# Kernel tuning notes

Hardware: AMD Instinct MI355X
Metric: run time of the kernel (lower is better)

## Reference

```python
import jax, jax.numpy as jnp
import numpy as np

LEAK = 0.2
NUM_GRAPHS = 64


def _gat(h_in, src, dst, eh, W, att_src, att_dst, att_edge, lin_edge_W, bias, N):
    # PyG GATConv with edge_dim, concat=False (mean over heads)
    H, C = att_src.shape
    h = (h_in @ W).reshape(N, H, C)                      # [N,H,C]
    e = (eh @ lin_edge_W).reshape(-1, H, C)              # [Eaug,H,C]
    a_s = jnp.einsum('nhc,hc->nh', h, att_src)           # [N,H]
    a_d = jnp.einsum('nhc,hc->nh', h, att_dst)
    a_e = jnp.einsum('ehc,hc->eh', e, att_edge)          # [Eaug,H]
    score = jax.nn.leaky_relu(a_s[src] + a_d[dst] + a_e, LEAK)
    # scatter-softmax over incoming edges of each destination node
    m = jax.ops.segment_max(score, dst, num_segments=N)
    ex = jnp.exp(score - m[dst])
    den = jax.ops.segment_sum(ex, dst, num_segments=N)
    alpha = ex / den[dst]                                # [Eaug,H]
    out = jax.ops.segment_sum(alpha[:, :, None] * h[src], dst, num_segments=N)
    return out.mean(axis=1) + bias                       # concat=False -> head mean


def setup_inputs() -> dict:
    key = jax.random.key(0)
    ks = jax.random.split(key, 32)
    N, E, F, FE, HID, H, NT = 30000, 480000, 64, 16, 64, 4, 16
    Cin1 = F + HID
    s = 0.05
    d = {
        'x': jax.random.normal(ks[0], (N, F), jnp.float32),
        'edge_attr': jax.random.normal(ks[1], (E, FE), jnp.float32),
        'node_emb': jax.random.normal(ks[2], (NT, HID), jnp.float32) * s,
        'edge_W': jax.random.normal(ks[3], (FE, HID), jnp.float32) * s,
        'edge_b': jnp.zeros((HID,), jnp.float32),
        'W1': jax.random.normal(ks[4], (Cin1, H * HID), jnp.float32) * s,
        'as1': jax.random.normal(ks[5], (H, HID), jnp.float32) * s,
        'ad1': jax.random.normal(ks[6], (H, HID), jnp.float32) * s,
        'ae1': jax.random.normal(ks[7], (H, HID), jnp.float32) * s,
        'leW1': jax.random.normal(ks[8], (HID, H * HID), jnp.float32) * s,
        'b1': jnp.zeros((HID,), jnp.float32),
        'W2': jax.random.normal(ks[9], (HID, H * HID), jnp.float32) * s,
        'as2': jax.random.normal(ks[10], (H, HID), jnp.float32) * s,
        'ad2': jax.random.normal(ks[11], (H, HID), jnp.float32) * s,
        'ae2': jax.random.normal(ks[12], (H, HID), jnp.float32) * s,
        'leW2': jax.random.normal(ks[13], (HID, H * HID), jnp.float32) * s,
        'b2': jnp.zeros((HID,), jnp.float32),
        'sage_Wl': jax.random.normal(ks[14], (HID, HID), jnp.float32) * s,
        'sage_bl': jnp.zeros((HID,), jnp.float32),
        'sage_Wr': jax.random.normal(ks[15], (HID, HID), jnp.float32) * s,
        'lin1_W': jax.random.normal(ks[16], (HID, HID), jnp.float32) * s,
        'lin1_b': jnp.zeros((HID,), jnp.float32),
        'lin2_W': jax.random.normal(ks[17], (HID, HID), jnp.float32) * s,
        'lin2_b': jnp.zeros((HID,), jnp.float32),
        'tel_W': jax.random.normal(ks[18], (HID, 1), jnp.float32) * s,
        'tel_b': jnp.zeros((1,), jnp.float32),
        'comp_W': jax.random.normal(ks[19], (HID, 1), jnp.float32) * s,
        'comp_b': jnp.zeros((1,), jnp.float32),
        'pch_W': jax.random.normal(ks[20], (HID, 1), jnp.float32) * s,
        'pch_b': jnp.zeros((1,), jnp.float32),
        'edge_index': jax.random.randint(ks[21], (2, E), 0, N, jnp.int32),
        'batch': jnp.sort(jax.random.randint(ks[22], (N,), 0, NUM_GRAPHS, jnp.int32)),
        'node_type': jax.random.randint(ks[23], (N,), 0, NT, jnp.int32),
    }
    return d


def reference(x, edge_attr, node_emb, edge_W, edge_b,
              W1, as1, ad1, ae1, leW1, b1,
              W2, as2, ad2, ae2, leW2, b2,
              sage_Wl, sage_bl, sage_Wr,
              lin1_W, lin1_b, lin2_W, lin2_b,
              tel_W, tel_b, comp_W, comp_b, pch_W, pch_b,
              edge_index, batch, node_type):
    N = x.shape[0]
    src0, dst0 = edge_index[0], edge_index[1]

    h0 = jnp.concatenate([x, node_emb[node_type]], axis=-1)   # [N, F+HID]
    eh = edge_attr @ edge_W + edge_b                          # [E, HID]

    # GATConv default add_self_loops=True, fill_value='mean' on edge_attr
    loop = jnp.arange(N, dtype=src0.dtype)
    src = jnp.concatenate([src0, loop])
    dst = jnp.concatenate([dst0, loop])
    eh_aug = jnp.concatenate([eh, jnp.broadcast_to(eh.mean(axis=0), (N, eh.shape[1]))], axis=0)

    h1 = jax.nn.elu(_gat(h0, src, dst, eh_aug, W1, as1, ad1, ae1, leW1, b1, N))
    h2 = jax.nn.elu(_gat(h1, src, dst, eh_aug, W2, as2, ad2, ae2, leW2, b2, N))

    # SAGEConv: mean neighbor aggregation (src->dst) + root transform
    deg = jax.ops.segment_sum(jnp.ones_like(dst0, dtype=h2.dtype), dst0, num_segments=N)
    agg = jax.ops.segment_sum(h2[src0], dst0, num_segments=N) / jnp.clip(deg, 1.0)[:, None]
    h3 = jax.nn.elu(agg @ sage_Wl + sage_bl + h2 @ sage_Wr)

    # global mean pool per graph
    cnt = jax.ops.segment_sum(jnp.ones((N,), h3.dtype), batch, num_segments=NUM_GRAPHS)
    g = jax.ops.segment_sum(h3, batch, num_segments=NUM_GRAPHS) / jnp.clip(cnt, 1.0)[:, None]

    g = jax.nn.elu(g @ lin1_W + lin1_b)                       # dropout inactive (eval)
    g = g @ lin2_W + lin2_b
    return (g @ tel_W + tel_b, g @ comp_W + comp_b, g @ pch_W + pch_b)
```

## Files before the change

kernel.cpp:

```cpp
#include <hip/hip_runtime.h>
#include <math.h>

#define NN 30000
#define NE 480000
#define FEA 16
#define HID 64
#define NG 64
#define LEAKK 0.2f

#define S_AEL1   0
#define S_AEL2   4
#define S_KF1    16
#define S_C1     80
#define S_KF2    88
#define S_C2     152
#define S_MS1    160
#define S_MD1    672
#define S_MS2    1184
#define S_MD2    1440

#define BT1H 0
#define BT1L 20480
#define BT2H 40960
#define BT2L 57344
#define BT3H 73728
#define BT3L 81920

typedef __attribute__((ext_vector_type(8))) short short8;
typedef __attribute__((ext_vector_type(4))) float f32x4;

__device__ __forceinline__ float eluf(float v) { return v > 0.f ? v : expm1f(v); }
__device__ __forceinline__ float leakyf(float v) { return v >= 0.f ? v : LEAKK * v; }
__device__ __forceinline__ void fma4(float4& a, float w, const float4& x) {
    a.x += w * x.x; a.y += w * x.y; a.z += w * x.z; a.w += w * x.w;
}
__device__ __forceinline__ unsigned bf16pack(float a, float b) {
    unsigned ua = __float_as_uint(a), ub = __float_as_uint(b);
    ua = (ua + 0x7FFFu + ((ua >> 16) & 1u)) >> 16;
    ub = (ub + 0x7FFFu + ((ub >> 16) & 1u)) >> 16;
    return ua | (ub << 16);
}
__device__ __forceinline__ unsigned short bf1(float v) {
    unsigned u = __float_as_uint(v);
    return (unsigned short)((u + 0x7FFFu + ((u >> 16) & 1u)) >> 16);
}
__device__ __forceinline__ float bf1tof(unsigned short h) {
    return __uint_as_float(((unsigned)h) << 16);
}
__device__ __forceinline__ uint2 bfpack4(float a, float b, float c, float d) {
    return make_uint2(bf16pack(a, b), bf16pack(c, d));
}
__device__ __forceinline__ float4 bf16x4(uint2 p) {
    float4 r;
    r.x = __uint_as_float(p.x << 16);
    r.y = __uint_as_float(p.x & 0xFFFF0000u);
    r.z = __uint_as_float(p.y << 16);
    r.w = __uint_as_float(p.y & 0xFFFF0000u);
    return r;
}
__device__ __forceinline__ float4 escore4(float4 a, float4 b, float4 c) {
    float4 r;
    r.x = expf(leakyf(a.x + b.x + c.x));
    r.y = expf(leakyf(a.y + b.y + c.y));
    r.z = expf(leakyf(a.z + b.z + c.z));
    r.w = expf(leakyf(a.w + b.w + c.w));
    return r;
}

__global__ __launch_bounds__(256) void cm_prepw_kernel(
    const int* __restrict__ dst, int* __restrict__ cnt, int* __restrict__ rank,
    const float* __restrict__ W1, const float* __restrict__ W2,
    const float* __restrict__ Wl, const float* __restrict__ Wr,
    const float* __restrict__ emb,
    const float* __restrict__ leW1, const float* __restrict__ aew1,
    const float* __restrict__ leW2, const float* __restrict__ aew2,
    const float* __restrict__ edge_W, const float* __restrict__ edge_b,
    const float* __restrict__ as1, const float* __restrict__ ad1,
    const float* __restrict__ as2, const float* __restrict__ ad2,
    const int* __restrict__ batch,
    unsigned short* __restrict__ BT,
    float* __restrict__ S, int* __restrict__ goff) {
    int t = threadIdx.x, bx = blockIdx.x;
    if (bx < 176) {
        int i = bx * 256 + t;
        float v = 0.f;
        int dsti = -1;
        if (i < 16384) {
            int kk = i >> 6, c = i & 63;
            int h = kk >> 6, k = kk & 63;
            v = 0.25f * W1[k * 256 + h * 64 + c];
            dsti = BT1H + c * 320 + kk;
        } else if (i < 20480) {
            int j2 = i - 16384;
            int r2 = j2 >> 6, c = j2 & 63;
            int tau = r2 >> 2, h = r2 & 3;
            float acc = 0.f;
            for (int j = 0; j < 64; j++)
                acc += emb[tau * 64 + j] * W1[(64 + j) * 256 + h * 64 + c];
            v = 0.25f * acc;
            dsti = BT1H + c * 320 + 256 + r2;
        } else if (i < 36864) {
            int j = i - 20480;
            int kk = j >> 6, c = j & 63;
            int h = kk >> 6, k = kk & 63;
            v = 0.25f * W2[k * 256 + h * 64 + c];
            dsti = BT2H + c * 256 + kk;
        } else if (i < 45056) {
            int j = i - 36864;
            int k = j >> 6, c = j & 63;
            v = (k < 64) ? Wl[k * 64 + c] : Wr[(k - 64) * 64 + c];
            dsti = BT3H + c * 128 + k;
        }
        if (dsti >= 0) {
            unsigned short hi = bf1(v);
            unsigned short lo = bf1(v - bf1tof(hi));
            BT[dsti] = hi;
            BT[dsti + 20480 - ((dsti >= BT2H) ? ((dsti >= BT3H) ? 12288 : 4096) : 0)] = lo;
        }
        return;
    }
    if (bx < 178) {
        int i = (bx - 176) * 256 + t;
        int k = i >> 2, h = i & 3;
        float s = 0.f, d = 0.f;
        for (int c = 0; c < 64; c++) {
            float w = W1[k * 256 + h * 64 + c];
            s += w * as1[h * 64 + c];
            d += w * ad1[h * 64 + c];
        }
        S[S_MS1 + i] = s; S[S_MD1 + i] = d;
        return;
    }
    if (bx == 178) {
        int k = t >> 2, h = t & 3;
        float s = 0.f, d = 0.f;
        for (int c = 0; c < 64; c++) {
            float w = W2[k * 256 + h * 64 + c];
            s += w * as2[h * 64 + c];
            d += w * ad2[h * 64 + c];
        }
        S[S_MS2 + t] = s; S[S_MD2 + t] = d;
        return;
    }
    if (bx == 179) {
        __shared__ float M1s[256], M2s[256];
        {
            int k = t >> 2, h = t & 3;
            float m1 = 0.f, m2 = 0.f;
            for (int c = 0; c < 64; c++) {
                m1 += leW1[k * 256 + h * 64 + c] * aew1[h * 64 + c];
                m2 += leW2[k * 256 + h * 64 + c] * aew2[h * 64 + c];
            }
            M1s[t] = m1; M2s[t] = m2;
        }
        __syncthreads();
        if (t < 64) {
            int f = t >> 2, h = t & 3;
            float k1 = 0.f, k2 = 0.f;
            for (int k = 0; k < 64; k++) {
                k1 += edge_W[f * 64 + k] * M1s[k * 4 + h];
                k2 += edge_W[f * 64 + k] * M2s[k * 4 + h];
            }
            S[S_KF1 + t] = k1; S[S_KF2 + t] = k2;
        } else if (t < 68) {
            int h = t - 64;
            float c1 = 0.f, c2 = 0.f;
            for (int k = 0; k < 64; k++) {
                c1 += edge_b[k] * M1s[k * 4 + h];
                c2 += edge_b[k] * M2s[k * 4 + h];
            }
            S[S_C1 + h] = c1; S[S_C2 + h] = c2;
        }
        return;
    }
    if (bx == 180) {
        if (t > NG) return;
        int lo = 0, hi = NN;
        while (lo < hi) {
            int mid = (lo + hi) >> 1;
            if (batch[mid] < t) lo = mid + 1; else hi = mid;
        }
        goff[t] = lo;
        return;
    }
    int e = (bx - 181) * 256 + t;
    if (e < NE) rank[e] = atomicAdd(&cnt[dst[e]], 1);
}

__global__ void scan_blocks_kernel(const int* __restrict__ cnt, int* __restrict__ eoff,
                                   int* __restrict__ bsum) {
    __shared__ int wsum[16];
    int t = threadIdx.x;
    int i = blockIdx.x * 1024 + t;
    int v = (i < NN) ? cnt[i] : 0;
    int lane = t & 63;
    int incl = v;
#pragma unroll
    for (int ofs = 1; ofs < 64; ofs <<= 1) {
        int u = __shfl_up(incl, ofs, 64);
        if (lane >= ofs) incl += u;
    }
    int wid = t >> 6;
    if (lane == 63) wsum[wid] = incl;
    __syncthreads();
    if (t < 16) {
        int s = wsum[t];
#pragma unroll
        for (int ofs = 1; ofs < 16; ofs <<= 1) {
            int u = __shfl_up(s, ofs, 64);
            if (t >= ofs) s += u;
        }
        wsum[t] = s;
    }
    __syncthreads();
    int excl = incl - v + (wid > 0 ? wsum[wid - 1] : 0);
    if (i < NN) eoff[i] = excl;
    if (t == 1023) bsum[blockIdx.x] = excl + v;
}

__global__ __launch_bounds__(256) void scanadd_attn_kernel(
    const int* __restrict__ bsum, int* __restrict__ eoff,
    const float* __restrict__ x, const float* __restrict__ node_emb,
    const int* __restrict__ node_type, const float* __restrict__ S,
    float* __restrict__ as_, float* __restrict__ ad_, unsigned* __restrict__ xb) {
    __shared__ float xt[64 * 132];
    __shared__ float ms[512], md[512];
    __shared__ int ntS[64];
    int t = threadIdx.x;
    if (blockIdx.x < 118) {
        int j = blockIdx.x >> 2;
        int pref = 0;
        for (int u = 0; u < j; u++) pref += bsum[u];
        int i = blockIdx.x * 256 + t;
        if (i < NN) eoff[i] += pref;
        if (i == 0) eoff[NN] = NE;
        return;
    }
    int n0 = (blockIdx.x - 118) * 64;
    if (t < 64) {
        int n = n0 + t;
        ntS[t] = (n < NN) ? node_type[n] : 0;
    }
    for (int i = t; i < 512; i += 256) { ms[i] = S[S_MS1 + i]; md[i] = S[S_MD1 + i]; }
    __syncthreads();
    for (int i = t; i < 1024; i += 256) {
        int r = i >> 4, c4 = (i & 15) * 4;
        int n = n0 + r;
        float4 f = {0, 0, 0, 0};
        if (n < NN) f = *(const float4*)(x + (size_t)n * 64 + c4);
        *(float4*)&xt[r * 132 + c4] = f;
    }
    for (int i = t; i < 1024; i += 256) {
        int r = i >> 4, c4 = (i & 15) * 4;
        int n = n0 + r;
        float4 f = {0, 0, 0, 0};
        if (n < NN) f = *(const float4*)(node_emb + (size_t)ntS[r] * 64 + c4);
        *(float4*)&xt[r * 132 + 64 + c4] = f;
    }
    __syncthreads();
    for (int i = t; i < 2048; i += 256) {
        int r = i >> 5, u = i & 31;
        int n = n0 + r;
        if (n < NN)
            xb[(size_t)n * 32 + u] = bf16pack(xt[r * 132 + 2 * u], xt[r * 132 + 2 * u + 1]);
    }
    int r = t >> 2, h = t & 3;
    float s = 0.f, d = 0.f;
#pragma unroll 8
    for (int k = 0; k < 128; k++) {
        float xv = xt[r * 132 + k];
        s += xv * ms[k * 4 + h];
        d += xv * md[k * 4 + h];
    }
    int n = n0 + r;
    if (n < NN) { as_[n * 4 + h] = s; ad_[n * 4 + h] = d; }
}

__global__ __launch_bounds__(256) void scatter_proj_kernel(
    const int* __restrict__ src, const int* __restrict__ dst,
    const float* __restrict__ EA, const float* __restrict__ S,
    const float* __restrict__ as_, const float* __restrict__ ad_,
    const int* __restrict__ node_type,
    const int* __restrict__ eoff, const int* __restrict__ rank,
    int* __restrict__ sep, int* __restrict__ dsrt,
    float4* __restrict__ sc1st, float4* __restrict__ ae2st,
    float* __restrict__ Ssum) {
    __shared__ float KF1s[64], KF2s[64], Cs[8];
    __shared__ float red[32];
    int t = threadIdx.x;
    if (t < 64) { KF1s[t] = S[S_KF1 + t]; KF2s[t] = S[S_KF2 + t]; }
    else if (t < 72) { int q = t - 64; Cs[q] = (q < 4) ? S[S_C1 + q] : S[S_C2 + q - 4]; }
    __syncthreads();
    int e = blockIdx.x * 256 + t;
    int s = src[e], d = dst[e];
    float a1[4], a2[4];
#pragma unroll
    for (int h = 0; h < 4; h++) { a1[h] = Cs[h]; a2[h] = Cs[4 + h]; }
    const float4* EA4 = (const float4*)(EA + (size_t)e * FEA);
#pragma unroll
    for (int q = 0; q < 4; q++) {
        float4 v = EA4[q];
        float vv[4] = {v.x, v.y, v.z, v.w};
#pragma unroll
        for (int j = 0; j < 4; j++) {
            int f = q * 4 + j;
#pragma unroll
            for (int h = 0; h < 4; h++) {
                a1[h] += vv[j] * KF1s[f * 4 + h];
                a2[h] += vv[j] * KF2s[f * 4 + h];
            }
        }
    }
    int pos = eoff[d] + rank[e];
    sep[pos] = s | (node_type[s] << 16);
    dsrt[pos] = d;
    float4 asv = ((const float4*)as_)[s];
    float4 adv = ((const float4*)ad_)[d];
    sc1st[pos] = escore4(asv, adv, make_float4(a1[0], a1[1], a1[2], a1[3]));
    ae2st[pos] = make_float4(a2[0], a2[1], a2[2], a2[3]);
    float v[8] = {a1[0], a1[1], a1[2], a1[3], a2[0], a2[1], a2[2], a2[3]};
#pragma unroll
    for (int mask = 1; mask < 64; mask <<= 1)
#pragma unroll
        for (int j = 0; j < 8; j++) v[j] += __shfl_xor(v[j], mask, 64);
    int lane = t & 63, wid = t >> 6;
    if (lane == 0)
#pragma unroll
        for (int j = 0; j < 8; j++) red[wid * 8 + j] = v[j];
    __syncthreads();
    if (t < 8) atomicAdd(&Ssum[t], red[t] + red[8 + t] + red[16 + t] + red[24 + t]);
}

__global__ __launch_bounds__(256) void score2_kernel(
    const int* __restrict__ sep, const int* __restrict__ dsrt,
    const float* __restrict__ as_, const float* __restrict__ ad_,
    float4* __restrict__ ae2st) {
    int p = blockIdx.x * 256 + threadIdx.x;
    int s = sep[p] & 0xFFFF;
    int d = dsrt[p];
    ae2st[p] = escore4(((const float4*)as_)[s], ((const float4*)ad_)[d], ae2st[p]);
}

__global__ __launch_bounds__(256) void agg_gat1_kernel(
    const int* __restrict__ eoff, const int* __restrict__ sep,
    const float* __restrict__ scs, const unsigned* __restrict__ xb,
    const int* __restrict__ node_type,
    const float* __restrict__ as_, const float* __restrict__ ad_,
    const float* __restrict__ S, uint2* __restrict__ aggb) {
    int n = blockIdx.x * 4 + (threadIdx.x >> 6);
    if (n >= NN) return;
    int lane = threadIdx.x & 63;
    int sub = lane >> 4, ch = lane & 15;
    const uint2* Xb = (const uint2*)xb;
    const float4* W4 = (const float4*)scs;
    float4 asn = ((const float4*)as_)[n];
    float4 adn = ((const float4*)ad_)[n];
    float4 a0 = {0, 0, 0, 0}, a1 = a0, a2 = a0, a3 = a0, dn = a0, tw = a0;
    int b = eoff[n], e_end = eoff[n + 1];
    int nE = e_end - b;
    int i = sub;
    for (; i + 4 < nE; i += 8) {
        int p0 = b + i, p1 = p0 + 4;
        int q0 = sep[p0], q1 = sep[p1];
        int s0 = q0 & 0xFFFF, t0 = q0 >> 16;
        int s1 = q1 & 0xFFFF, t1 = q1 >> 16;
        float4 w0 = W4[p0], w1 = W4[p1];
        float4 x0 = bf16x4(Xb[(size_t)s0 * 16 + ch]);
        float4 x1 = bf16x4(Xb[(size_t)s1 * 16 + ch]);
        fma4(a0, w0.x, x0); fma4(a1, w0.y, x0); fma4(a2, w0.z, x0); fma4(a3, w0.w, x0);
        fma4(a0, w1.x, x1); fma4(a1, w1.y, x1); fma4(a2, w1.z, x1); fma4(a3, w1.w, x1);
        dn.x += w0.x + w1.x; dn.y += w0.y + w1.y;
        dn.z += w0.z + w1.z; dn.w += w0.w + w1.w;
        if (ch == t0) { tw.x += w0.x; tw.y += w0.y; tw.z += w0.z; tw.w += w0.w; }
        if (ch == t1) { tw.x += w1.x; tw.y += w1.y; tw.z += w1.z; tw.w += w1.w; }
    }
    for (; i < nE; i += 4) {
        int p0 = b + i;
        int q0 = sep[p0];
        int s0 = q0 & 0xFFFF, t0 = q0 >> 16;
        float4 w0 = W4[p0];
        float4 x0 = bf16x4(Xb[(size_t)s0 * 16 + ch]);
        fma4(a0, w0.x, x0); fma4(a1, w0.y, x0); fma4(a2, w0.z, x0); fma4(a3, w0.w, x0);
        dn.x += w0.x; dn.y += w0.y; dn.z += w0.z; dn.w += w0.w;
        if (ch == t0) { tw.x += w0.x; tw.y += w0.y; tw.z += w0.z; tw.w += w0.w; }
    }
    if (sub == 0) {
        const float inv = 1.f / (float)NE;
        float e0 = expf(leakyf(asn.x + adn.x + S[S_AEL1 + 0] * inv));
        float e1 = expf(leakyf(asn.y + adn.y + S[S_AEL1 + 1] * inv));
        float e2 = expf(leakyf(asn.z + adn.z + S[S_AEL1 + 2] * inv));
        float e3 = expf(leakyf(asn.w + adn.w + S[S_AEL1 + 3] * inv));
        float4 xs = bf16x4(Xb[(size_t)n * 16 + ch]);
        fma4(a0, e0, xs); fma4(a1, e1, xs); fma4(a2, e2, xs); fma4(a3, e3, xs);
        dn.x += e0; dn.y += e1; dn.z += e2; dn.w += e3;
        int tn = node_type[n];
        if (ch == tn) { tw.x += e0; tw.y += e1; tw.z += e2; tw.w += e3; }
    }
#pragma unroll
    for (int mask = 16; mask < 64; mask <<= 1) {
        a0.x += __shfl_xor(a0.x, mask, 64); a0.y += __shfl_xor(a0.y, mask, 64);
        a0.z += __shfl_xor(a0.z, mask, 64); a0.w += __shfl_xor(a0.w, mask, 64);
        a1.x += __shfl_xor(a1.x, mask, 64); a1.y += __shfl_xor(a1.y, mask, 64);
        a1.z += __shfl_xor(a1.z, mask, 64); a1.w += __shfl_xor(a1.w, mask, 64);
        a2.x += __shfl_xor(a2.x, mask, 64); a2.y += __shfl_xor(a2.y, mask, 64);
        a2.z += __shfl_xor(a2.z, mask, 64); a2.w += __shfl_xor(a2.w, mask, 64);
        a3.x += __shfl_xor(a3.x, mask, 64); a3.y += __shfl_xor(a3.y, mask, 64);
        a3.z += __shfl_xor(a3.z, mask, 64); a3.w += __shfl_xor(a3.w, mask, 64);
        dn.x += __shfl_xor(dn.x, mask, 64); dn.y += __shfl_xor(dn.y, mask, 64);
        dn.z += __shfl_xor(dn.z, mask, 64); dn.w += __shfl_xor(dn.w, mask, 64);
        tw.x += __shfl_xor(tw.x, mask, 64); tw.y += __shfl_xor(tw.y, mask, 64);
        tw.z += __shfl_xor(tw.z, mask, 64); tw.w += __shfl_xor(tw.w, mask, 64);
    }
    if (sub == 0) {
        float i0 = 1.f / dn.x, i1 = 1.f / dn.y, i2 = 1.f / dn.z, i3 = 1.f / dn.w;
        uint2* A2 = aggb + (size_t)n * 80;
        A2[ch]      = bfpack4(a0.x * i0, a0.y * i0, a0.z * i0, a0.w * i0);
        A2[16 + ch] = bfpack4(a1.x * i1, a1.y * i1, a1.z * i1, a1.w * i1);
        A2[32 + ch] = bfpack4(a2.x * i2, a2.y * i2, a2.z * i2, a2.w * i2);
        A2[48 + ch] = bfpack4(a3.x * i3, a3.y * i3, a3.z * i3, a3.w * i3);
        A2[64 + ch] = bfpack4(tw.x * i0, tw.y * i1, tw.z * i2, tw.w * i3);
    }
}

__global__ __launch_bounds__(256) void agg_gat2_kernel(
    const int* __restrict__ eoff, const int* __restrict__ sep,
    const float* __restrict__ w2s, const unsigned* __restrict__ h1b,
    const float* __restrict__ as_, const float* __restrict__ ad_,
    const float* __restrict__ S, uint2* __restrict__ aggb) {
    int n = blockIdx.x * 4 + (threadIdx.x >> 6);
    if (n >= NN) return;
    int lane = threadIdx.x & 63;
    int sub = lane >> 4, ch = lane & 15;
    const uint2* Xb = (const uint2*)h1b;
    const float4* W4 = (const float4*)w2s;
    float4 asn = ((const float4*)as_)[n];
    float4 adn = ((const float4*)ad_)[n];
    float4 a0 = {0, 0, 0, 0}, a1 = a0, a2 = a0, a3 = a0, dn = a0;
    int b = eoff[n], e = eoff[n + 1];
    int nE = e - b;
    int i = sub;
    for (; i + 4 < nE; i += 8) {
        int p0 = b + i, p1 = p0 + 4;
        int s0 = sep[p0] & 0xFFFF, s1 = sep[p1] & 0xFFFF;
        float4 w0 = W4[p0], w1 = W4[p1];
        float4 x0 = bf16x4(Xb[(size_t)s0 * 16 + ch]);
        float4 x1 = bf16x4(Xb[(size_t)s1 * 16 + ch]);
        fma4(a0, w0.x, x0); fma4(a1, w0.y, x0); fma4(a2, w0.z, x0); fma4(a3, w0.w, x0);
        fma4(a0, w1.x, x1); fma4(a1, w1.y, x1); fma4(a2, w1.z, x1); fma4(a3, w1.w, x1);
        dn.x += w0.x + w1.x; dn.y += w0.y + w1.y;
        dn.z += w0.z + w1.z; dn.w += w0.w + w1.w;
    }
    for (; i < nE; i += 4) {
        int p0 = b + i;
        int s0 = sep[p0] & 0xFFFF;
        float4 w0 = W4[p0];
        float4 x0 = bf16x4(Xb[(size_t)s0 * 16 + ch]);
        fma4(a0, w0.x, x0); fma4(a1, w0.y, x0); fma4(a2, w0.z, x0); fma4(a3, w0.w, x0);
        dn.x += w0.x; dn.y += w0.y; dn.z += w0.z; dn.w += w0.w;
    }
    if (sub == 0) {
        const float inv = 1.f / (float)NE;
        float e0 = expf(leakyf(asn.x + adn.x + S[S_AEL2 + 0] * inv));
        float e1 = expf(leakyf(asn.y + adn.y + S[S_AEL2 + 1] * inv));
        float e2 = expf(leakyf(asn.z + adn.z + S[S_AEL2 + 2] * inv));
        float e3 = expf(leakyf(asn.w + adn.w + S[S_AEL2 + 3] * inv));
        float4 xs = bf16x4(Xb[(size_t)n * 16 + ch]);
        fma4(a0, e0, xs); fma4(a1, e1, xs); fma4(a2, e2, xs); fma4(a3, e3, xs);
        dn.x += e0; dn.y += e1; dn.z += e2; dn.w += e3;
    }
#pragma unroll
    for (int mask = 16; mask < 64; mask <<= 1) {
        a0.x += __shfl_xor(a0.x, mask, 64); a0.y += __shfl_xor(a0.y, mask, 64);
        a0.z += __shfl_xor(a0.z, mask, 64); a0.w += __shfl_xor(a0.w, mask, 64);
        a1.x += __shfl_xor(a1.x, mask, 64); a1.y += __shfl_xor(a1.y, mask, 64);
        a1.z += __shfl_xor(a1.z, mask, 64); a1.w += __shfl_xor(a1.w, mask, 64);
        a2.x += __shfl_xor(a2.x, mask, 64); a2.y += __shfl_xor(a2.y, mask, 64);
        a2.z += __shfl_xor(a2.z, mask, 64); a2.w += __shfl_xor(a2.w, mask, 64);
        a3.x += __shfl_xor(a3.x, mask, 64); a3.y += __shfl_xor(a3.y, mask, 64);
        a3.z += __shfl_xor(a3.z, mask, 64); a3.w += __shfl_xor(a3.w, mask, 64);
        dn.x += __shfl_xor(dn.x, mask, 64); dn.y += __shfl_xor(dn.y, mask, 64);
        dn.z += __shfl_xor(dn.z, mask, 64); dn.w += __shfl_xor(dn.w, mask, 64);
    }
    if (sub == 0) {
        float i0 = 1.f / dn.x, i1 = 1.f / dn.y, i2 = 1.f / dn.z, i3 = 1.f / dn.w;
        uint2* A2 = aggb + (size_t)n * 64;
        A2[ch]      = bfpack4(a0.x * i0, a0.y * i0, a0.z * i0, a0.w * i0);
        A2[16 + ch] = bfpack4(a1.x * i1, a1.y * i1, a1.z * i1, a1.w * i1);
        A2[32 + ch] = bfpack4(a2.x * i2, a2.y * i2, a2.z * i2, a2.w * i2);
        A2[48 + ch] = bfpack4(a3.x * i3, a3.y * i3, a3.z * i3, a3.w * i3);
    }
}

template <int K, bool DOATT>
__global__ __launch_bounds__(256) void gemm_mfma_kernel(
    const unsigned* __restrict__ A, const unsigned short* __restrict__ bth,
    const unsigned short* __restrict__ btl,
    const float* __restrict__ bias, float* __restrict__ out,
    unsigned short* __restrict__ out16,
    const float* __restrict__ ms_g, const float* __restrict__ md_g,
    float* __restrict__ as_, float* __restrict__ ad_) {
    int t = threadIdx.x;
    int w = t >> 6, l = t & 63;
    int lr = l & 15, lg = l >> 4;
    int m0 = blockIdx.x * 64 + w * 16;
    int am = m0 + lr;
    bool av = am < NN;
    const short8* Arow = (const short8*)A + (size_t)am * (K / 8);
    short8 zz = {0, 0, 0, 0, 0, 0, 0, 0};
    f32x4 acc[4];
#pragma unroll
    for (int ct = 0; ct < 4; ct++) acc[ct] = (f32x4){0.f, 0.f, 0.f, 0.f};
#pragma unroll
    for (int k0 = 0; k0 < K; k0 += 32) {
        short8 a = av ? Arow[(k0 >> 3) + lg] : zz;
#pragma unroll
        for (int ct = 0; ct < 4; ct++) {
            int bo = (ct * 16 + lr) * K + k0 + lg * 8;
            short8 bh = *(const short8*)(bth + bo);
            short8 bl = *(const short8*)(btl + bo);
            acc[ct] = __builtin_amdgcn_mfma_f32_16x16x32_bf16(a, bh, acc[ct], 0, 0, 0);
            acc[ct] = __builtin_amdgcn_mfma_f32_16x16x32_bf16(a, bl, acc[ct], 0, 0, 0);
        }
    }
    f32x4 ps[4], pd[4];
    if (DOATT) {
#pragma unroll
        for (int r = 0; r < 4; r++) {
            ps[r] = (f32x4){0.f, 0.f, 0.f, 0.f};
            pd[r] = (f32x4){0.f, 0.f, 0.f, 0.f};
        }
    }
#pragma unroll
    for (int ct = 0; ct < 4; ct++) {
        int col = ct * 16 + lr;
        float bv = bias[col];
        f32x4 ms4, md4;
        if (DOATT) {
            ms4 = ((const f32x4*)ms_g)[col];
            md4 = ((const f32x4*)md_g)[col];
        }
#pragma unroll
        for (int r = 0; r < 4; r++) {
            int m = m0 + lg * 4 + r;
            float o = eluf(acc[ct][r] + bv);
            if (m < NN) {
                if (out) out[(size_t)m * 64 + col] = o;
                if (out16) out16[(size_t)m * 64 + col] = bf1(o);
            }
            if (DOATT) { ps[r] += o * ms4; pd[r] += o * md4; }
        }
    }
    if (DOATT) {
#pragma unroll
        for (int mk = 1; mk < 16; mk <<= 1)
#pragma unroll
            for (int r = 0; r < 4; r++) {
                ps[r][0] += __shfl_xor(ps[r][0], mk, 64);
                ps[r][1] += __shfl_xor(ps[r][1], mk, 64);
                ps[r][2] += __shfl_xor(ps[r][2], mk, 64);
                ps[r][3] += __shfl_xor(ps[r][3], mk, 64);
                pd[r][0] += __shfl_xor(pd[r][0], mk, 64);
                pd[r][1] += __shfl_xor(pd[r][1], mk, 64);
                pd[r][2] += __shfl_xor(pd[r][2], mk, 64);
                pd[r][3] += __shfl_xor(pd[r][3], mk, 64);
            }
        if (lr == 0) {
#pragma unroll
            for (int r = 0; r < 4; r++) {
                int m = m0 + lg * 4 + r;
                if (m < NN) {
                    *(f32x4*)(as_ + (size_t)m * 4) = ps[r];
                    *(f32x4*)(ad_ + (size_t)m * 4) = pd[r];
                }
            }
        }
    }
}

__global__ __launch_bounds__(256) void sage_agg3_kernel(
    const unsigned* __restrict__ h2b,
    const int* __restrict__ eoff, const int* __restrict__ sep,
    uint2* __restrict__ AB) {
    int n = blockIdx.x * 16 + (threadIdx.x >> 4);
    if (n >= NN) return;
    int l = threadIdx.x & 15;
    const uint2* Hb = (const uint2*)h2b;
    float ax = 0.f, ay = 0.f, az = 0.f, aw = 0.f;
    int b = eoff[n], e_end = eoff[n + 1];
    int idx = b;
    int stop = b + ((e_end - b) & ~7);
    if (idx < stop) {
        int sreg[8];
#pragma unroll
        for (int u = 0; u < 8; u++) sreg[u] = sep[idx + u] & 0xFFFF;
        idx += 8;
        while (true) {
            int sn[8];
            bool more = idx < stop;
            if (more) {
#pragma unroll
                for (int u = 0; u < 8; u++) sn[u] = sep[idx + u] & 0xFFFF;
            }
#pragma unroll
            for (int u = 0; u < 8; u++) {
                float4 v = bf16x4(Hb[(size_t)sreg[u] * 16 + l]);
                ax += v.x; ay += v.y; az += v.z; aw += v.w;
            }
            if (!more) break;
#pragma unroll
            for (int u = 0; u < 8; u++) sreg[u] = sn[u];
            idx += 8;
        }
    }
    for (; idx < e_end; idx++) {
        float4 v0 = bf16x4(Hb[(size_t)(sep[idx] & 0xFFFF) * 16 + l]);
        ax += v0.x; ay += v0.y; az += v0.z; aw += v0.w;
    }
    float dg = (float)(e_end - b);
    if (dg < 1.f) dg = 1.f;
    float inv = 1.f / dg;
    AB[(size_t)n * 32 + l] = bfpack4(ax * inv, ay * inv, az * inv, aw * inv);
    AB[(size_t)n * 32 + 16 + l] = Hb[(size_t)n * 16 + l];
}

__global__ __launch_bounds__(256) void pool_mlp_kernel(
    const float* __restrict__ h3, const int* __restrict__ goff,
    const float* __restrict__ lin1W, const float* __restrict__ lin1b,
    const float* __restrict__ lin2W, const float* __restrict__ lin2b,
    const float* __restrict__ telW, const float* __restrict__ telb,
    const float* __restrict__ compW, const float* __restrict__ compb,
    const float* __restrict__ pchW, const float* __restrict__ pchb,
    float* __restrict__ out) {
    __shared__ float red[256];
    __shared__ float g[64], G1[64], G2[64];
    int gi = blockIdx.x, t = threadIdx.x;
    int c = t & 63, li = t >> 6;
    int b = goff[gi], e = goff[gi + 1];
    float sum = 0.f;
    for (int r = b + li; r < e; r += 4) sum += h3[(size_t)r * HID + c];
    red[t] = sum;
    __syncthreads();
    if (t < 64) {
        float v = red[t] + red[t + 64] + red[t + 128] + red[t + 192];
        float cntf = (float)(e - b);
        if (cntf < 1.f) cntf = 1.f;
        g[t] = v / cntf;
    }
    __syncthreads();
    {
        float part = 0.f;
#pragma unroll
        for (int k = li * 16; k < li * 16 + 16; k++) part += g[k] * lin1W[k * 64 + c];
        red[t] = part;
        __syncthreads();
        if (t < 64)
            G1[c] = eluf(red[c] + red[c + 64] + red[c + 128] + red[c + 192] + lin1b[c]);
        __syncthreads();
    }
    {
        float part = 0.f;
#pragma unroll
        for (int k = li * 16; k < li * 16 + 16; k++) part += G1[k] * lin2W[k * 64 + c];
        red[t] = part;
        __syncthreads();
        if (t < 64)
            G2[c] = red[c] + red[c + 64] + red[c + 128] + red[c + 192] + lin2b[c];
        __syncthreads();
    }
    if (t < 192) {
        int h = t >> 6, k = t & 63;
        const float* W = (h == 0) ? telW : ((h == 1) ? compW : pchW);
        red[t] = G2[k] * W[k];
    }
    __syncthreads();
    if (t < 3) {
        float acc = 0.f;
        for (int k = 0; k < 64; k++) acc += red[t * 64 + k];
        float bb = (t == 0) ? telb[0] : ((t == 1) ? compb[0] : pchb[0]);
        out[t * 64 + gi] = acc + bb;
    }
}

extern "C" void kernel_launch(void* const* d_in, const int* in_sizes, int n_in,
                              void* d_out, int out_size, void* d_ws, size_t ws_size,
                              hipStream_t stream) {
    const float* x        = (const float*)d_in[0];
    const float* EA       = (const float*)d_in[1];
    const float* node_emb = (const float*)d_in[2];
    const float* edge_W   = (const float*)d_in[3];
    const float* edge_b   = (const float*)d_in[4];
    const float* W1       = (const float*)d_in[5];
    const float* as1      = (const float*)d_in[6];
    const float* ad1      = (const float*)d_in[7];
    const float* ae1      = (const float*)d_in[8];
    const float* leW1     = (const float*)d_in[9];
    const float* b1       = (const float*)d_in[10];
    const float* W2       = (const float*)d_in[11];
    const float* as2      = (const float*)d_in[12];
    const float* ad2      = (const float*)d_in[13];
    const float* ae2      = (const float*)d_in[14];
    const float* leW2     = (const float*)d_in[15];
    const float* b2       = (const float*)d_in[16];
    const float* sage_Wl  = (const float*)d_in[17];
    const float* sage_bl  = (const float*)d_in[18];
    const float* sage_Wr  = (const float*)d_in[19];
    const float* lin1_W   = (const float*)d_in[20];
    const float* lin1_b   = (const float*)d_in[21];
    const float* lin2_W   = (const float*)d_in[22];
    const float* lin2_b   = (const float*)d_in[23];
    const float* tel_W    = (const float*)d_in[24];
    const float* tel_b    = (const float*)d_in[25];
    const float* comp_W   = (const float*)d_in[26];
    const float* comp_b   = (const float*)d_in[27];
    const float* pch_W    = (const float*)d_in[28];
    const float* pch_b    = (const float*)d_in[29];
    const int* edge_index = (const int*)d_in[30];
    const int* batch      = (const int*)d_in[31];
    const int* node_type  = (const int*)d_in[32];
    float* outp = (float*)d_out;

    const int* srcp = edge_index;
    const int* dstp = edge_index + NE;

    float* wf = (float*)d_ws;
    constexpr size_t OFF_H3    = 0;
    constexpr size_t OFF_AGG   = OFF_H3 + (size_t)NN * 64;
    constexpr size_t OFF_SC1   = OFF_AGG + (size_t)NN * 512;
    constexpr size_t OFF_H2    = OFF_SC1 + (size_t)NE * 4;
    constexpr size_t OFF_SC    = OFF_H2 + (size_t)NN * 64;
    constexpr size_t OFF_AE2   = OFF_SC + (size_t)NE * 4;
    constexpr size_t OFF_AS    = OFF_AE2 + (size_t)NE * 4;
    constexpr size_t OFF_AD    = OFF_AS + (size_t)NN * 4;
    constexpr size_t OFF_SMALL = OFF_AD + (size_t)NN * 4;
    constexpr size_t OFF_BT    = OFF_SMALL + 4096;
    constexpr size_t OFF_XB    = OFF_BT + 45056;
    constexpr size_t OFF_H1B   = OFF_XB + (size_t)NN * 32;
    constexpr size_t OFF_H2B   = OFF_H1B + (size_t)NN * 32;
    constexpr size_t F_TOTAL   = OFF_H2B + (size_t)NN * 32;

    int* wi   = (int*)(wf + F_TOTAL);
    int* cnt  = wi;
    int* rank = wi + NN;
    int* eoff = rank + NE;
    int* sep  = eoff + (NN + 2);
    int* dsrt = sep + NE;
    int* goff = dsrt + NE;
    int* bsum = goff + (NG + 1);

    float* h3    = wf + OFF_H3;
    float* aggb  = wf + OFF_AGG;
    float* sc1st = wf + OFF_SC1;
    float* ae2st = wf + OFF_AE2;
    float* as_   = wf + OFF_AS;
    float* ad_   = wf + OFF_AD;
    float* S     = wf + OFF_SMALL;
    unsigned short* BT = (unsigned short*)(wf + OFF_BT);
    unsigned* xb  = (unsigned*)(wf + OFF_XB);
    unsigned short* h1b = (unsigned short*)(wf + OFF_H1B);
    unsigned short* h2b = (unsigned short*)(wf + OFF_H2B);

    hipMemsetAsync(S, 0, 16 * sizeof(float), stream);
    hipMemsetAsync(cnt, 0, NN * sizeof(int), stream);

    cm_prepw_kernel<<<181 + (NE + 255) / 256, 256, 0, stream>>>(
        dstp, cnt, rank, W1, W2, sage_Wl, sage_Wr, node_emb,
        leW1, ae1, leW2, ae2, edge_W, edge_b, as1, ad1, as2, ad2, batch,
        BT, S, goff);

    scan_blocks_kernel<<<(NN + 1023) / 1024, 1024, 0, stream>>>(cnt, eoff, bsum);
    scanadd_attn_kernel<<<118 + (NN + 63) / 64, 256, 0, stream>>>(
        bsum, eoff, x, node_emb, node_type, S, as_, ad_, xb);

    scatter_proj_kernel<<<NE / 256, 256, 0, stream>>>(
        srcp, dstp, EA, S, as_, ad_, node_type, eoff, rank,
        sep, dsrt, (float4*)sc1st, (float4*)ae2st, S);

    agg_gat1_kernel<<<(NN + 3) / 4, 256, 0, stream>>>(
        eoff, sep, sc1st, xb, node_type, as_, ad_, S, (uint2*)aggb);
    gemm_mfma_kernel<320, true><<<(NN + 63) / 64, 256, 0, stream>>>(
        (const unsigned*)aggb, BT + BT1H, BT + BT1L, b1, nullptr, h1b,
        S + S_MS2, S + S_MD2, as_, ad_);

    score2_kernel<<<NE / 256, 256, 0, stream>>>(sep, dsrt, as_, ad_, (float4*)ae2st);
    agg_gat2_kernel<<<(NN + 3) / 4, 256, 0, stream>>>(
        eoff, sep, ae2st, (const unsigned*)h1b, as_, ad_, S, (uint2*)aggb);
    gemm_mfma_kernel<256, false><<<(NN + 63) / 64, 256, 0, stream>>>(
        (const unsigned*)aggb, BT + BT2H, BT + BT2L, b2, nullptr, h2b,
        nullptr, nullptr, nullptr, nullptr);

    sage_agg3_kernel<<<(NN + 15) / 16, 256, 0, stream>>>(
        (const unsigned*)h2b, eoff, sep, (uint2*)aggb);
    gemm_mfma_kernel<128, false><<<(NN + 63) / 64, 256, 0, stream>>>(
        (const unsigned*)aggb, BT + BT3H, BT + BT3L, sage_bl, h3, nullptr,
        nullptr, nullptr, nullptr, nullptr);

    pool_mlp_kernel<<<NG, 256, 0, stream>>>(h3, goff, lin1_W, lin1_b, lin2_W, lin2_b,
                                            tel_W, tel_b, comp_W, comp_b, pch_W, pch_b, outp);
}
```

Measured before the change: 386.0 us.

## Pack per-edge scores and indices into 32-byte fp16 records

Replaces the separate per-edge arrays (sep, dsrt, fp32 layer-1 scores, fp32 layer-2 edge terms) with one interleaved 32-byte record per sorted edge. The record holds the fp16 layer-1 weights, the fp16 layer-2 edge term (later overwritten with the layer-2 weights), the packed source/type index and the destination. The aim is to turn several scattered loads and stores into fewer, co-located 16-byte accesses and to halve the score storage. In exchange the exp weights lose precision in fp16, the aggregation kernels read 8 of every 32 bytes for the weights with a stride, and score2 writes a compact sepc array for the SAGE pass.

```diff
diff --git a/kernel.cpp b/kernel.cpp
--- a/kernel.cpp
+++ b/kernel.cpp
@@ -1,4 +1,5 @@
 #include <hip/hip_runtime.h>
+#include <hip/hip_fp16.h>
 #include <math.h>
 
 #define NN 30000
@@ -58,6 +59,18 @@
     r.w = __uint_as_float(p.y & 0xFFFF0000u);
     return r;
 }
+__device__ __forceinline__ unsigned h2pack(float a, float b) {
+    __half2 h = __floats2half2_rn(a, b);
+    return *(unsigned*)&h;
+}
+__device__ __forceinline__ float2 h2unpack(unsigned u) {
+    __half2 h = *(__half2*)&u;
+    return __half22float2(h);
+}
+__device__ __forceinline__ float4 h4tof(uint2 p) {
+    float2 lo = h2unpack(p.x), hi = h2unpack(p.y);
+    return make_float4(lo.x, lo.y, hi.x, hi.y);
+}
 __device__ __forceinline__ float4 escore4(float4 a, float4 b, float4 c) {
     float4 r;
     r.x = expf(leakyf(a.x + b.x + c.x));
@@ -66,6 +79,7 @@
     r.w = expf(leakyf(a.w + b.w + c.w));
     return r;
 }
+
 
 __global__ __launch_bounds__(256) void cm_prepw_kernel(
     const int* __restrict__ dst, int* __restrict__ cnt, int* __restrict__ rank,
@@ -282,9 +296,7 @@
     const float* __restrict__ as_, const float* __restrict__ ad_,
     const int* __restrict__ node_type,
     const int* __restrict__ eoff, const int* __restrict__ rank,
-    int* __restrict__ sep, int* __restrict__ dsrt,
-    float4* __restrict__ sc1st, float4* __restrict__ ae2st,
-    float* __restrict__ Ssum) {
+    uint4* __restrict__ recs, float* __restrict__ Ssum) {
     __shared__ float KF1s[64], KF2s[64], Cs[8];
     __shared__ float red[32];
     int t = threadIdx.x;
@@ -312,12 +324,14 @@
         }
     }
     int pos = eoff[d] + rank[e];
-    sep[pos] = s | (node_type[s] << 16);
-    dsrt[pos] = d;
     float4 asv = ((const float4*)as_)[s];
     float4 adv = ((const float4*)ad_)[d];
-    sc1st[pos] = escore4(asv, adv, make_float4(a1[0], a1[1], a1[2], a1[3]));
-    ae2st[pos] = make_float4(a2[0], a2[1], a2[2], a2[3]);
+    float4 w1 = escore4(asv, adv, make_float4(a1[0], a1[1], a1[2], a1[3]));
+    uint4 lo = make_uint4(h2pack(w1.x, w1.y), h2pack(w1.z, w1.w),
+                          h2pack(a2[0], a2[1]), h2pack(a2[2], a2[3]));
+    uint4 hi = make_uint4((unsigned)(s | (node_type[s] << 16)), (unsigned)d, 0u, 0u);
+    recs[2 * pos] = lo;
+    recs[2 * pos + 1] = hi;
     float v[8] = {a1[0], a1[1], a1[2], a1[3], a2[0], a2[1], a2[2], a2[3]};
 #pragma unroll
     for (int mask = 1; mask < 64; mask <<= 1)
@@ -332,18 +346,21 @@
 }
 
 __global__ __launch_bounds__(256) void score2_kernel(
-    const int* __restrict__ sep, const int* __restrict__ dsrt,
+    uint4* __restrict__ recs,
     const float* __restrict__ as_, const float* __restrict__ ad_,
-    float4* __restrict__ ae2st) {
+    int* __restrict__ sepc) {
     int p = blockIdx.x * 256 + threadIdx.x;
-    int s = sep[p] & 0xFFFF;
-    int d = dsrt[p];
-    ae2st[p] = escore4(((const float4*)as_)[s], ((const float4*)ad_)[d], ae2st[p]);
+    uint2 a2h = ((const uint2*)recs)[4 * p + 1];
+    int2 sd = ((const int2*)recs)[4 * p + 2];
+    int s = sd.x & 0xFFFF;
+    float4 w2 = escore4(((const float4*)as_)[s], ((const float4*)ad_)[sd.y], h4tof(a2h));
+    ((uint2*)recs)[4 * p + 1] = make_uint2(h2pack(w2.x, w2.y), h2pack(w2.z, w2.w));
+    sepc[p] = sd.x;
 }
 
 __global__ __launch_bounds__(256) void agg_gat1_kernel(
-    const int* __restrict__ eoff, const int* __restrict__ sep,
-    const float* __restrict__ scs, const unsigned* __restrict__ xb,
+    const int* __restrict__ eoff, const uint4* __restrict__ recs,
+    const unsigned* __restrict__ xb,
     const int* __restrict__ node_type,
     const float* __restrict__ as_, const float* __restrict__ ad_,
     const float* __restrict__ S, uint2* __restrict__ aggb) {
@@ -352,7 +369,8 @@
     int lane = threadIdx.x & 63;
     int sub = lane >> 4, ch = lane & 15;
     const uint2* Xb = (const uint2*)xb;
-    const float4* W4 = (const float4*)scs;
+    const int* RI = (const int*)recs;
+    const uint2* RW = (const uint2*)recs;
     float4 asn = ((const float4*)as_)[n];
     float4 adn = ((const float4*)ad_)[n];
     float4 a0 = {0, 0, 0, 0}, a1 = a0, a2 = a0, a3 = a0, dn = a0, tw = a0;
@@ -361,10 +379,10 @@
     int i = sub;
     for (; i + 4 < nE; i += 8) {
         int p0 = b + i, p1 = p0 + 4;
-        int q0 = sep[p0], q1 = sep[p1];
+        int q0 = RI[8 * p0 + 4], q1 = RI[8 * p1 + 4];
         int s0 = q0 & 0xFFFF, t0 = q0 >> 16;
         int s1 = q1 & 0xFFFF, t1 = q1 >> 16;
-        float4 w0 = W4[p0], w1 = W4[p1];
+        float4 w0 = h4tof(RW[4 * p0]), w1 = h4tof(RW[4 * p1]);
         float4 x0 = bf16x4(Xb[(size_t)s0 * 16 + ch]);
         float4 x1 = bf16x4(Xb[(size_t)s1 * 16 + ch]);
         fma4(a0, w0.x, x0); fma4(a1, w0.y, x0); fma4(a2, w0.z, x0); fma4(a3, w0.w, x0);
@@ -376,9 +394,9 @@
     }
     for (; i < nE; i += 4) {
         int p0 = b + i;
-        int q0 = sep[p0];
+        int q0 = RI[8 * p0 + 4];
         int s0 = q0 & 0xFFFF, t0 = q0 >> 16;
-        float4 w0 = W4[p0];
+        float4 w0 = h4tof(RW[4 * p0]);
         float4 x0 = bf16x4(Xb[(size_t)s0 * 16 + ch]);
         fma4(a0, w0.x, x0); fma4(a1, w0.y, x0); fma4(a2, w0.z, x0); fma4(a3, w0.w, x0);
         dn.x += w0.x; dn.y += w0.y; dn.z += w0.z; dn.w += w0.w;
@@ -423,8 +441,8 @@
 }
 
 __global__ __launch_bounds__(256) void agg_gat2_kernel(
-    const int* __restrict__ eoff, const int* __restrict__ sep,
-    const float* __restrict__ w2s, const unsigned* __restrict__ h1b,
+    const int* __restrict__ eoff, const uint4* __restrict__ recs,
+    const unsigned* __restrict__ h1b,
     const float* __restrict__ as_, const float* __restrict__ ad_,
     const float* __restrict__ S, uint2* __restrict__ aggb) {
     int n = blockIdx.x * 4 + (threadIdx.x >> 6);
@@ -432,7 +450,8 @@
     int lane = threadIdx.x & 63;
     int sub = lane >> 4, ch = lane & 15;
     const uint2* Xb = (const uint2*)h1b;
-    const float4* W4 = (const float4*)w2s;
+    const int* RI = (const int*)recs;
+    const uint2* RW = (const uint2*)recs;
     float4 asn = ((const float4*)as_)[n];
     float4 adn = ((const float4*)ad_)[n];
     float4 a0 = {0, 0, 0, 0}, a1 = a0, a2 = a0, a3 = a0, dn = a0;
@@ -441,8 +460,8 @@
     int i = sub;
     for (; i + 4 < nE; i += 8) {
         int p0 = b + i, p1 = p0 + 4;
-        int s0 = sep[p0] & 0xFFFF, s1 = sep[p1] & 0xFFFF;
-        float4 w0 = W4[p0], w1 = W4[p1];
+        int s0 = RI[8 * p0 + 4] & 0xFFFF, s1 = RI[8 * p1 + 4] & 0xFFFF;
+        float4 w0 = h4tof(RW[4 * p0 + 1]), w1 = h4tof(RW[4 * p1 + 1]);
         float4 x0 = bf16x4(Xb[(size_t)s0 * 16 + ch]);
         float4 x1 = bf16x4(Xb[(size_t)s1 * 16 + ch]);
         fma4(a0, w0.x, x0); fma4(a1, w0.y, x0); fma4(a2, w0.z, x0); fma4(a3, w0.w, x0);
@@ -452,8 +471,8 @@
     }
     for (; i < nE; i += 4) {
         int p0 = b + i;
-        int s0 = sep[p0] & 0xFFFF;
-        float4 w0 = W4[p0];
+        int s0 = RI[8 * p0 + 4] & 0xFFFF;
+        float4 w0 = h4tof(RW[4 * p0 + 1]);
         float4 x0 = bf16x4(Xb[(size_t)s0 * 16 + ch]);
         fma4(a0, w0.x, x0); fma4(a1, w0.y, x0); fma4(a2, w0.z, x0); fma4(a3, w0.w, x0);
         dn.x += w0.x; dn.y += w0.y; dn.z += w0.z; dn.w += w0.w;
@@ -579,7 +598,7 @@
 
 __global__ __launch_bounds__(256) void sage_agg3_kernel(
     const unsigned* __restrict__ h2b,
-    const int* __restrict__ eoff, const int* __restrict__ sep,
+    const int* __restrict__ eoff, const int* __restrict__ sepc,
     uint2* __restrict__ AB) {
     int n = blockIdx.x * 16 + (threadIdx.x >> 4);
     if (n >= NN) return;
@@ -592,14 +611,14 @@
     if (idx < stop) {
         int sreg[8];
 #pragma unroll
-        for (int u = 0; u < 8; u++) sreg[u] = sep[idx + u] & 0xFFFF;
+        for (int u = 0; u < 8; u++) sreg[u] = sepc[idx + u] & 0xFFFF;
         idx += 8;
         while (true) {
             int sn[8];
             bool more = idx < stop;
             if (more) {
 #pragma unroll
-                for (int u = 0; u < 8; u++) sn[u] = sep[idx + u] & 0xFFFF;
+                for (int u = 0; u < 8; u++) sn[u] = sepc[idx + u] & 0xFFFF;
             }
 #pragma unroll
             for (int u = 0; u < 8; u++) {
@@ -613,7 +632,7 @@
         }
     }
     for (; idx < e_end; idx++) {
-        float4 v0 = bf16x4(Hb[(size_t)(sep[idx] & 0xFFFF) * 16 + l]);
+        float4 v0 = bf16x4(Hb[(size_t)(sepc[idx] & 0xFFFF) * 16 + l]);
         ax += v0.x; ay += v0.y; az += v0.z; aw += v0.w;
     }
     float dg = (float)(e_end - b);
@@ -725,11 +744,8 @@
     float* wf = (float*)d_ws;
     constexpr size_t OFF_H3    = 0;
     constexpr size_t OFF_AGG   = OFF_H3 + (size_t)NN * 64;
-    constexpr size_t OFF_SC1   = OFF_AGG + (size_t)NN * 512;
-    constexpr size_t OFF_H2    = OFF_SC1 + (size_t)NE * 4;
-    constexpr size_t OFF_SC    = OFF_H2 + (size_t)NN * 64;
-    constexpr size_t OFF_AE2   = OFF_SC + (size_t)NE * 4;
-    constexpr size_t OFF_AS    = OFF_AE2 + (size_t)NE * 4;
+    constexpr size_t OFF_REC   = OFF_AGG + (size_t)NN * 512;
+    constexpr size_t OFF_AS    = OFF_REC + (size_t)NE * 8;
     constexpr size_t OFF_AD    = OFF_AS + (size_t)NN * 4;
     constexpr size_t OFF_SMALL = OFF_AD + (size_t)NN * 4;
     constexpr size_t OFF_BT    = OFF_SMALL + 4096;
@@ -742,15 +758,13 @@
     int* cnt  = wi;
     int* rank = wi + NN;
     int* eoff = rank + NE;
-    int* sep  = eoff + (NN + 2);
-    int* dsrt = sep + NE;
-    int* goff = dsrt + NE;
+    int* sepc = eoff + (NN + 2);
+    int* goff = sepc + NE;
     int* bsum = goff + (NG + 1);
 
     float* h3    = wf + OFF_H3;
     float* aggb  = wf + OFF_AGG;
-    float* sc1st = wf + OFF_SC1;
-    float* ae2st = wf + OFF_AE2;
+    uint4* recs  = (uint4*)(wf + OFF_REC);
     float* as_   = wf + OFF_AS;
     float* ad_   = wf + OFF_AD;
     float* S     = wf + OFF_SMALL;
@@ -772,24 +786,23 @@
         bsum, eoff, x, node_emb, node_type, S, as_, ad_, xb);
 
     scatter_proj_kernel<<<NE / 256, 256, 0, stream>>>(
-        srcp, dstp, EA, S, as_, ad_, node_type, eoff, rank,
-        sep, dsrt, (float4*)sc1st, (float4*)ae2st, S);
+        srcp, dstp, EA, S, as_, ad_, node_type, eoff, rank, recs, S);
 
     agg_gat1_kernel<<<(NN + 3) / 4, 256, 0, stream>>>(
-        eoff, sep, sc1st, xb, node_type, as_, ad_, S, (uint2*)aggb);
+        eoff, recs, xb, node_type, as_, ad_, S, (uint2*)aggb);
     gemm_mfma_kernel<320, true><<<(NN + 63) / 64, 256, 0, stream>>>(
         (const unsigned*)aggb, BT + BT1H, BT + BT1L, b1, nullptr, h1b,
         S + S_MS2, S + S_MD2, as_, ad_);
 
-    score2_kernel<<<NE / 256, 256, 0, stream>>>(sep, dsrt, as_, ad_, (float4*)ae2st);
+    score2_kernel<<<NE / 256, 256, 0, stream>>>(recs, as_, ad_, sepc);
     agg_gat2_kernel<<<(NN + 3) / 4, 256, 0, stream>>>(
-        eoff, sep, ae2st, (const unsigned*)h1b, as_, ad_, S, (uint2*)aggb);
+        eoff, recs, (const unsigned*)h1b, as_, ad_, S, (uint2*)aggb);
     gemm_mfma_kernel<256, false><<<(NN + 63) / 64, 256, 0, stream>>>(
         (const unsigned*)aggb, BT + BT2H, BT + BT2L, b2, nullptr, h2b,
         nullptr, nullptr, nullptr, nullptr);
 
     sage_agg3_kernel<<<(NN + 15) / 16, 256, 0, stream>>>(
-        (const unsigned*)h2b, eoff, sep, (uint2*)aggb);
+        (const unsigned*)h2b, eoff, sepc, (uint2*)aggb);
     gemm_mfma_kernel<128, false><<<(NN + 63) / 64, 256, 0, stream>>>(
         (const unsigned*)aggb, BT + BT3H, BT + BT3L, sage_bl, h3, nullptr,
         nullptr, nullptr, nullptr, nullptr);
```

After: 378.8 us. No clear change (-1.9%).
